# Performance work log

Measured on AMD Instinct MI355X. Metric: run time of the kernel, lower is better.

## Reference

```python
import jax, jax.numpy as jnp
import numpy as np


def ternary_quantize(w):
    # threshold = 0.7 * mean(|w|); maps w to {-1, 0, +1}
    threshold = 0.7 * jnp.sum(jnp.abs(w)) / w.size
    return jnp.sign(jnp.sign(w + threshold) + jnp.sign(w - threshold))


def setup_inputs() -> dict:
    key = jax.random.key(0)
    k1, k2, k3 = jax.random.split(key, 3)
    B, N = 4096, 8192
    x = jax.random.normal(k1, (B, N), dtype=jnp.float32)
    kernel = jax.random.normal(k2, (N,), dtype=jnp.float32)
    bias = jax.random.normal(k3, (N,), dtype=jnp.float32)
    return {"x": x, "kernel": kernel, "bias": bias}


def reference(x, kernel, bias):
    # Original: y = x @ diag(ternary(kernel)) + bias.
    # Matmul by a diagonal matrix is exactly a per-column scale; we compute
    # the identical math as a fused elementwise scale + bias add.
    q = ternary_quantize(kernel)          # [N] in {-1, 0, 1}
    return x * q[None, :] + bias[None, :]  # [B, N]
```

## Files before the change

### kernel.cpp

```cpp
#include <hip/hip_runtime.h>

typedef float f32x4 __attribute__((ext_vector_type(4)));

__global__ __launch_bounds__(256) void fused_ternary_scale_bias(
    const f32x4* __restrict__ x, const float* __restrict__ w,
    const f32x4* __restrict__ bias4, f32x4* __restrict__ out,
    int n, long total4) {
    __shared__ float red[256];
    const int tid = threadIdx.x;

    float s = 0.f;
    for (int i = tid; i < n; i += 256) s += fabsf(w[i]);
    red[tid] = s;
    __syncthreads();
    for (int off = 128; off > 0; off >>= 1) {
        if (tid < off) red[tid] += red[tid + off];
        __syncthreads();
    }
    const float t = 0.7f * red[0] / (float)n;

    const int n4 = n >> 2;
    const long i0 = (long)blockIdx.x * blockDim.x + tid;
    const long stride = (long)gridDim.x * blockDim.x;
    const int c = (int)(i0 & (long)(n4 - 1));

    const f32x4 wv = reinterpret_cast<const f32x4*>(w)[c];
    f32x4 qv;
    qv.x = (fabsf(wv.x) >= t) ? copysignf(1.f, wv.x) : 0.f;
    qv.y = (fabsf(wv.y) >= t) ? copysignf(1.f, wv.y) : 0.f;
    qv.z = (fabsf(wv.z) >= t) ? copysignf(1.f, wv.z) : 0.f;
    qv.w = (fabsf(wv.w) >= t) ? copysignf(1.f, wv.w) : 0.f;
    const f32x4 bv = bias4[c];

    for (long i = i0; i < total4; i += stride) {
        f32x4 xv = __builtin_nontemporal_load(&x[i]);
        f32x4 o = xv * qv + bv;
        __builtin_nontemporal_store(o, &out[i]);
    }
}

extern "C" void kernel_launch(void* const* d_in, const int* in_sizes, int n_in,
                              void* d_out, int out_size, void* d_ws, size_t ws_size,
                              hipStream_t stream) {
    const float* x      = (const float*)d_in[0];
    const float* kernel = (const float*)d_in[1];
    const float* bias   = (const float*)d_in[2];
    float* out = (float*)d_out;

    const int N = in_sizes[1];
    const long total4 = (long)out_size / 4;

    fused_ternary_scale_bias<<<2048, 256, 0, stream>>>(
        (const f32x4*)x, kernel, (const f32x4*)bias, (f32x4*)out, N, total4);
}
```

Baseline: 54.58 us.

## Specialize kernel for fixed shape, prefetch x before threshold reduction

Adds a fast path for N=8192 with a fixed 16-iteration unrolled loop. It issues the first four x loads before computing the mean-abs threshold, so the per-block reduction over the kernel vector overlaps with memory latency. The reduction itself is vectorized and uses wave shuffles instead of a shared-memory tree. The generic path is kept for other shapes, and the fast path is hardcoded to the test dimensions.

```diff
diff --git a/kernel.cpp b/kernel.cpp
--- a/kernel.cpp
+++ b/kernel.cpp
@@ -2,13 +2,73 @@
 
 typedef float f32x4 __attribute__((ext_vector_type(4)));
 
-__global__ __launch_bounds__(256) void fused_ternary_scale_bias(
+__device__ __forceinline__ f32x4 nt_load(const f32x4* p) {
+    return __builtin_nontemporal_load(p);
+}
+__device__ __forceinline__ void nt_store(f32x4 v, f32x4* p) {
+    __builtin_nontemporal_store(v, p);
+}
+
+__device__ __forceinline__ float tern(float w, float t) {
+    return (fabsf(w) >= t) ? copysignf(1.f, w) : 0.f;
+}
+
+template <int ITERS>
+__global__ __launch_bounds__(256) void fused_fast(
+    const f32x4* __restrict__ x, const float* __restrict__ w,
+    const f32x4* __restrict__ bias4, f32x4* __restrict__ out, int n) {
+    const int tid = threadIdx.x;
+    const int n4 = n >> 2;
+    const long stride = (long)gridDim.x * 256;
+    const long i0 = (long)blockIdx.x * 256 + tid;
+    const int c = (int)(i0 & (long)(n4 - 1));
+    const f32x4* w4 = reinterpret_cast<const f32x4*>(w);
+
+    f32x4 x0 = nt_load(&x[i0 + 0 * stride]);
+    f32x4 x1 = nt_load(&x[i0 + 1 * stride]);
+    f32x4 x2 = nt_load(&x[i0 + 2 * stride]);
+    f32x4 x3 = nt_load(&x[i0 + 3 * stride]);
+    const f32x4 wq = w4[c];
+    const f32x4 bv = bias4[c];
+
+    float s = 0.f;
+    #pragma unroll
+    for (int k = 0; k < 8; ++k) {
+        const f32x4 wv = w4[tid + k * 256];
+        s += fabsf(wv.x) + fabsf(wv.y) + fabsf(wv.z) + fabsf(wv.w);
+    }
+    #pragma unroll
+    for (int off = 32; off > 0; off >>= 1) s += __shfl_xor(s, off, 64);
+    __shared__ float partial[4];
+    if ((tid & 63) == 0) partial[tid >> 6] = s;
+    __syncthreads();
+    const float t = 0.7f * (partial[0] + partial[1] + partial[2] + partial[3])
+                    / (float)n;
+
+    f32x4 qv;
+    qv.x = tern(wq.x, t);
+    qv.y = tern(wq.y, t);
+    qv.z = tern(wq.z, t);
+    qv.w = tern(wq.w, t);
+
+    nt_store(x0 * qv + bv, &out[i0 + 0 * stride]);
+    nt_store(x1 * qv + bv, &out[i0 + 1 * stride]);
+    nt_store(x2 * qv + bv, &out[i0 + 2 * stride]);
+    nt_store(x3 * qv + bv, &out[i0 + 3 * stride]);
+
+    #pragma unroll
+    for (int k = 4; k < ITERS; ++k) {
+        const f32x4 xv = nt_load(&x[i0 + (long)k * stride]);
+        nt_store(xv * qv + bv, &out[i0 + (long)k * stride]);
+    }
+}
+
+__global__ __launch_bounds__(256) void fused_generic(
     const f32x4* __restrict__ x, const float* __restrict__ w,
     const f32x4* __restrict__ bias4, f32x4* __restrict__ out,
     int n, long total4) {
     __shared__ float red[256];
     const int tid = threadIdx.x;
-
     float s = 0.f;
     for (int i = tid; i < n; i += 256) s += fabsf(w[i]);
     red[tid] = s;
@@ -18,24 +78,19 @@
         __syncthreads();
     }
     const float t = 0.7f * red[0] / (float)n;
-
     const int n4 = n >> 2;
     const long i0 = (long)blockIdx.x * blockDim.x + tid;
     const long stride = (long)gridDim.x * blockDim.x;
-    const int c = (int)(i0 & (long)(n4 - 1));
-
-    const f32x4 wv = reinterpret_cast<const f32x4*>(w)[c];
-    f32x4 qv;
-    qv.x = (fabsf(wv.x) >= t) ? copysignf(1.f, wv.x) : 0.f;
-    qv.y = (fabsf(wv.y) >= t) ? copysignf(1.f, wv.y) : 0.f;
-    qv.z = (fabsf(wv.z) >= t) ? copysignf(1.f, wv.z) : 0.f;
-    qv.w = (fabsf(wv.w) >= t) ? copysignf(1.f, wv.w) : 0.f;
-    const f32x4 bv = bias4[c];
-
     for (long i = i0; i < total4; i += stride) {
-        f32x4 xv = __builtin_nontemporal_load(&x[i]);
-        f32x4 o = xv * qv + bv;
-        __builtin_nontemporal_store(o, &out[i]);
+        const int c = (int)(i % n4);
+        const f32x4 wv = reinterpret_cast<const f32x4*>(w)[c];
+        f32x4 qv;
+        qv.x = tern(wv.x, t);
+        qv.y = tern(wv.y, t);
+        qv.z = tern(wv.z, t);
+        qv.w = tern(wv.w, t);
+        const f32x4 bvv = bias4[c];
+        nt_store(x[i] * qv + bvv, &out[i]);
     }
 }
 
@@ -50,6 +105,16 @@
     const int N = in_sizes[1];
     const long total4 = (long)out_size / 4;
 
-    fused_ternary_scale_bias<<<2048, 256, 0, stream>>>(
-        (const f32x4*)x, kernel, (const f32x4*)bias, (f32x4*)out, N, total4);
+    constexpr int ITERS = 16;
+    const long stride = 2048L * 256;
+    if (N == 8192 && total4 == stride * ITERS) {
+        fused_fast<ITERS><<<2048, 256, 0, stream>>>(
+            (const f32x4*)x, kernel, (const f32x4*)bias, (f32x4*)out, N);
+    } else {
+        long blocks = (total4 + 255) / 256;
+        if (blocks > 2048) blocks = 2048;
+        fused_generic<<<(int)blocks, 256, 0, stream>>>(
+            (const f32x4*)x, kernel, (const f32x4*)bias, (f32x4*)out,
+            N, total4);
+    }
 }
```

Measured after the change: 68.68 us. +25.8%, slower.
